# Kernel optimization log

Hardware: AMD Instinct MI355X
Metric: run time of the kernel (lower is better)

## Reference

```python
import jax, jax.numpy as jnp
import numpy as np

N_NODES = 50000
EMB = 256
HEADS = 2
N_BASE_EDGES = 100000


def setup_inputs() -> dict:
    key = jax.random.key(0)
    ks = jax.random.split(key, 12)
    x = jax.random.normal(ks[0], (N_NODES, EMB), dtype=jnp.float32)
    # bipartite edges: sources in left half, targets in right half -> no self-loops
    src = jax.random.randint(ks[1], (N_BASE_EDGES,), 0, N_NODES // 2)
    dst = jax.random.randint(ks[2], (N_BASE_EDGES,), N_NODES // 2, N_NODES)
    edge_index = jnp.stack([src, dst]).astype(jnp.int64)
    hd = EMB // HEADS
    s = 0.02
    params = {
        "Wkqv": jax.random.normal(ks[3], (EMB, 3 * EMB), dtype=jnp.float32) * s,
        "bkqv": jnp.zeros((3 * EMB,), dtype=jnp.float32),
        "W1": jax.random.normal(ks[4], (2 * hd, hd), dtype=jnp.float32) * s,
        "b1": jnp.zeros((hd,), dtype=jnp.float32),
        "W2": jax.random.normal(ks[5], (hd, 1), dtype=jnp.float32) * s,
        "b2": jnp.zeros((1,), dtype=jnp.float32),
        "Wout": jax.random.normal(ks[6], (EMB, EMB), dtype=jnp.float32) * s,
        "bout": jnp.zeros((EMB,), dtype=jnp.float32),
    }
    return {"x": x, "edge_index": edge_index, **params}


def reference(x, edge_index, Wkqv, bkqv, W1, b1, W2, b2, Wout, bout):
    N, emb = x.shape
    H = HEADS
    hd = emb // H
    # MetaGNNNoEdgeAttr.forward preprocessing: make undirected + self loops.
    # Input is bipartite (no self-loops), so remove_self_loops is a no-op.
    ei = jnp.concatenate([edge_index, edge_index[::-1]], axis=1)
    loops = jnp.arange(N, dtype=edge_index.dtype)
    src = jnp.concatenate([ei[0], loops])  # j (message source)
    dst = jnp.concatenate([ei[1], loops])  # i (message target / softmax index)

    # single GNN layer (n_layers=1)
    kqv = x @ Wkqv + bkqv  # [N, 3*emb]
    q = kqv[dst, :emb].reshape(-1, H, hd)                                  # [E,H,hd]
    k = kqv[src, emb:2 * emb].reshape(-1, H, hd) / jnp.sqrt(jnp.float32(hd))
    v = kqv[src, 2 * emb:].reshape(-1, H, hd)

    h = jax.nn.relu(jnp.concatenate([k, q], axis=-1) @ W1 + b1)  # [E,H,hd]
    a = (h @ W2 + b2).squeeze(-1)                                # [E,H]

    # segment softmax over destination nodes (every node has a self-loop)
    m = jax.ops.segment_max(a, dst, num_segments=N)              # [N,H]
    ex = jnp.exp(a - m[dst])
    s = jax.ops.segment_sum(ex, dst, num_segments=N)             # [N,H]
    alpha = ex / (s[dst] + 1e-16)                                # [E,H]

    msg = (alpha[..., None] * v).reshape(-1, emb) @ Wout + bout  # [E,emb]
    out = jax.ops.segment_sum(msg, dst, num_segments=N)          # [N,emb]
    return jax.nn.relu(out) + x
```

## Files before the change

kernel.cpp:

```cpp
#include <hip/hip_runtime.h>
#include <hip/hip_bf16.h>

#define EMB 256

typedef __bf16 bf16_t;
typedef __attribute__((ext_vector_type(8))) __bf16 bf16x8;
typedef __attribute__((ext_vector_type(4))) __bf16 bf16x4;
typedef __attribute__((ext_vector_type(4))) float floatx4;

__device__ __forceinline__ int eidx(const int* __restrict__ p, int is64, long long k){
  return is64 ? p[2*k] : p[(int)k];
}
__device__ __forceinline__ void async_load16(const void* g, void* l){
  __builtin_amdgcn_global_load_lds(
      (const __attribute__((address_space(1))) unsigned int*)g,
      (__attribute__((address_space(3))) unsigned int*)l,
      16, 0, 0);
}
__device__ __forceinline__ float4 cvt4(bf16x4 v){
  return make_float4((float)v.x, (float)v.y, (float)v.z, (float)v.w);
}

__global__ void detect_kernel(const int* __restrict__ ei, int* __restrict__ flag){
  int z = (ei[1]==0) + (ei[3]==0) + (ei[5]==0) + (ei[7]==0);
  *flag = (z == 4) ? 1 : 0;
}

__global__ void prep_weights(const float* __restrict__ Wkqv, const float* __restrict__ bkqv,
                             const float* __restrict__ W1,
                             bf16_t* __restrict__ WcombT, float* __restrict__ bcomb){
  int n = blockIdx.x * blockDim.x + threadIdx.x;
  int c = blockIdx.y;
  if (n >= 768) return;
  const float rs = rsqrtf(128.0f);
  bool isBias = (c == 256);
  const float* arow = isBias ? bkqv : (Wkqv + (size_t)c*768);
  float val;
  if (n < 512){
    bool isQ = (n < 256);
    int nn = isQ ? n : (n - 256);
    int h = nn >> 7, d = nn & 127;
    int srcoff = isQ ? (h*128) : (256 + h*128);
    int w1off  = isQ ? 128 : 0;
    float s = 0.f;
    for (int t = 0; t < 128; ++t)
      s = fmaf(arow[srcoff + t], W1[(size_t)(w1off + t)*128 + d], s);
    val = isQ ? s : s * rs;
  } else {
    val = arow[512 + (n - 512)];
  }
  if (isBias) bcomb[n] = val;
  else        WcombT[(size_t)n*256 + c] = (bf16_t)val;
}

__global__ void prep_wout(const float* __restrict__ W, bf16_t* __restrict__ Wt){
  int t = blockIdx.x*blockDim.x + threadIdx.x;
  int n = t & 255, c = t >> 8;
  Wt[(size_t)n*256 + c] = (bf16_t)W[(size_t)c*256 + n];
}

__global__ void deg_kernel(const int* __restrict__ ei, const int* __restrict__ flag,
                           int* __restrict__ deg, int E0, int Nn){
  int t = blockIdx.x*blockDim.x + threadIdx.x;
  if (t >= 2*E0) return;
  int is64 = *flag;
  int i = (t < E0) ? eidx(ei,is64,(long long)E0+t) : eidx(ei,is64,t-E0);
  i = min(max(i,0), Nn-1);
  atomicAdd(deg + i, 1);
}

__global__ __launch_bounds__(1024) void scan_kernel(const int* __restrict__ deg,
                                                    int* __restrict__ off, int N){
  __shared__ int wsum[16];
  __shared__ int carry_s;
  int tid = threadIdx.x, lane = tid & 63, w = tid >> 6;
  if (tid == 0) carry_s = 0;
  __syncthreads();
  for (int base = 0; base < N; base += 1024){
    int carry = carry_s;
    int v = (base + tid < N) ? (deg[base + tid] + 1) : 0;
    int incl = v;
    #pragma unroll
    for (int o = 1; o < 64; o <<= 1){
      int t = __shfl_up(incl, o, 64);
      if (lane >= o) incl += t;
    }
    if (lane == 63) wsum[w] = incl;
    __syncthreads();
    if (w == 0 && lane < 16){
      int sv = wsum[lane];
      #pragma unroll
      for (int o = 1; o < 16; o <<= 1){
        int t = __shfl_up(sv, o, 64);
        if (lane >= o) sv += t;
      }
      wsum[lane] = sv;
    }
    __syncthreads();
    int wpref = (w == 0) ? 0 : wsum[w-1];
    if (base + tid < N) off[base + tid] = carry + wpref + incl - v;
    __syncthreads();
    if (tid == 1023) carry_s = carry + wsum[15];
    __syncthreads();
  }
  if (threadIdx.x == 0) off[N] = carry_s;
}

__global__ void scatter_kernel(const int* __restrict__ ei, const int* __restrict__ flag,
                               const int* __restrict__ off, int* __restrict__ cursor,
                               int* __restrict__ bj, int E0, int Nn){
  int e = blockIdx.x*blockDim.x + threadIdx.x;
  int E = 2*E0 + Nn;
  if (e >= E) return;
  int is64 = *flag;
  int j, i;
  if (e < E0){ j = eidx(ei,is64,e); i = eidx(ei,is64,(long long)E0+e); }
  else if (e < 2*E0){ int t = e - E0; i = eidx(ei,is64,t); j = eidx(ei,is64,(long long)E0+t); }
  else { i = j = e - 2*E0; }
  i = min(max(i,0), Nn-1); j = min(max(j,0), Nn-1);
  int pos = atomicAdd(cursor + i, 1);
  bj[off[i] + pos] = j;
}

template<int MODE, typename OutT>
__global__ __launch_bounds__(256) void mfma_gemm(
    const void* __restrict__ Av, const bf16_t* __restrict__ Bt,
    const float* __restrict__ bias, OutT* __restrict__ C,
    int M, int N,
    const int* __restrict__ deg, const float* __restrict__ xres)
{
  __shared__ bf16_t As[2][128*32];
  __shared__ bf16_t Bs[2][128*32];
  const int tid = threadIdx.x;
  const int wave = tid >> 6, lane = tid & 63;
  const int row16 = lane & 15, quad = lane >> 4;

  const int nn = N >> 7;
  const int bid = blockIdx.x;
  const int strip = bid / (8*nn);
  const int inner = bid % (8*nn);
  const int m0 = (strip*8 + (inner & 7)) * 128;
  const int n0 = (inner >> 3) * 128;
  const int wm = (wave >> 1) * 64, wn = (wave & 1) * 64;

  const float*  Af = (const float*)Av;
  const bf16_t* Ab = (const bf16_t*)Av;

  const int f0 = wave*2, f1 = wave*2 + 1;
  const int gm0 = min(m0 + f0*16 + row16, M-1);
  const int gm1 = min(m0 + f1*16 + row16, M-1);
  const int gn0 = n0 + f0*16 + row16;
  const int gn1 = n0 + f1*16 + row16;

  if (MODE == 0){
    const float* g0 = Af + (size_t)gm0*256 + quad*8;
    const float* g1 = Af + (size_t)gm1*256 + quad*8;
    float4 a0 = *(const float4*)g0, a1 = *(const float4*)(g0+4);
    float4 c0 = *(const float4*)g1, c1 = *(const float4*)(g1+4);
    bf16x8 v0 = {(bf16_t)a0.x,(bf16_t)a0.y,(bf16_t)a0.z,(bf16_t)a0.w,
                 (bf16_t)a1.x,(bf16_t)a1.y,(bf16_t)a1.z,(bf16_t)a1.w};
    bf16x8 v1 = {(bf16_t)c0.x,(bf16_t)c0.y,(bf16_t)c0.z,(bf16_t)c0.w,
                 (bf16_t)c1.x,(bf16_t)c1.y,(bf16_t)c1.z,(bf16_t)c1.w};
    *(bf16x8*)((char*)As[0] + f0*1024 + lane*16) = v0;
    *(bf16x8*)((char*)As[0] + f1*1024 + lane*16) = v1;
  } else {
    async_load16(Ab + (size_t)gm0*256 + quad*8, (char*)As[0] + f0*1024);
    async_load16(Ab + (size_t)gm1*256 + quad*8, (char*)As[0] + f1*1024);
  }
  async_load16(Bt + (size_t)gn0*256 + quad*8, (char*)Bs[0] + f0*1024);
  async_load16(Bt + (size_t)gn1*256 + quad*8, (char*)Bs[0] + f1*1024);

  floatx4 acc[4][4];
  #pragma unroll
  for (int a=0;a<4;++a)
    #pragma unroll
    for (int b=0;b<4;++b) acc[a][b] = (floatx4){0.f,0.f,0.f,0.f};

  #pragma unroll
  for (int kt = 0; kt < 8; ++kt){
    const int cur = kt & 1, nxt = cur ^ 1;
    const int k1 = (kt+1)*32;
    const bool pre = (kt < 7);
    float4 p0, p1, p2, p3;

    __syncthreads();

    if (pre){
      if (MODE == 0){
        const float* g0 = Af + (size_t)gm0*256 + k1 + quad*8;
        const float* g1 = Af + (size_t)gm1*256 + k1 + quad*8;
        p0 = *(const float4*)g0; p1 = *(const float4*)(g0+4);
        p2 = *(const float4*)g1; p3 = *(const float4*)(g1+4);
      } else {
        async_load16(Ab + (size_t)gm0*256 + k1 + quad*8, (char*)As[nxt] + f0*1024);
        async_load16(Ab + (size_t)gm1*256 + k1 + quad*8, (char*)As[nxt] + f1*1024);
      }
      async_load16(Bt + (size_t)gn0*256 + k1 + quad*8, (char*)Bs[nxt] + f0*1024);
      async_load16(Bt + (size_t)gn1*256 + k1 + quad*8, (char*)Bs[nxt] + f1*1024);
    }

    bf16x8 af[4], bfr[4];
    #pragma unroll
    for (int t = 0; t < 4; ++t){
      af[t]  = *(const bf16x8*)((const char*)As[cur] + ((wm>>4)+t)*1024 + lane*16);
      bfr[t] = *(const bf16x8*)((const char*)Bs[cur] + ((wn>>4)+t)*1024 + lane*16);
    }
    #pragma unroll
    for (int mt=0;mt<4;++mt)
      #pragma unroll
      for (int nt=0;nt<4;++nt)
        acc[mt][nt] = __builtin_amdgcn_mfma_f32_16x16x32_bf16(af[mt], bfr[nt], acc[mt][nt], 0,0,0);

    if (pre && MODE == 0){
      bf16x8 v0 = {(bf16_t)p0.x,(bf16_t)p0.y,(bf16_t)p0.z,(bf16_t)p0.w,
                   (bf16_t)p1.x,(bf16_t)p1.y,(bf16_t)p1.z,(bf16_t)p1.w};
      bf16x8 v1 = {(bf16_t)p2.x,(bf16_t)p2.y,(bf16_t)p2.z,(bf16_t)p2.w,
                   (bf16_t)p3.x,(bf16_t)p3.y,(bf16_t)p3.z,(bf16_t)p3.w};
      *(bf16x8*)((char*)As[nxt] + f0*1024 + lane*16) = v0;
      *(bf16x8*)((char*)As[nxt] + f1*1024 + lane*16) = v1;
    }
  }

  #pragma unroll
  for (int mt=0;mt<4;++mt){
    #pragma unroll
    for (int r=0;r<4;++r){
      int m = m0 + wm + mt*16 + quad*4 + r;
      if (m >= M) continue;
      float dg = (MODE==1) ? (float)(deg[m]+1) : 0.f;
      #pragma unroll
      for (int nt=0;nt<4;++nt){
        int n = n0 + wn + nt*16 + row16;
        float v = acc[mt][nt][r];
        if (MODE == 0){
          v += bias[n];
        } else {
          v = fmaxf(v + dg*bias[n], 0.f) + xres[(size_t)m*N + n];
        }
        C[(size_t)m*N + n] = (OutT)v;
      }
    }
  }
}

__global__ __launch_bounds__(256) void fused_attn_kernel(
    const bf16_t* __restrict__ P, const int* __restrict__ bj, const int* __restrict__ off,
    const float* __restrict__ b1, const float* __restrict__ W2, const float* __restrict__ b2,
    bf16_t* __restrict__ aggb, int Nn)
{
  int i = blockIdx.x * (blockDim.x >> 6) + (threadIdx.x >> 6);
  if (i >= Nn) return;
  int lane = threadIdx.x & 63;
  int h = lane >> 5, d = (lane & 31) * 4;

  const float4 qv  = cvt4(*(const bf16x4*)(P + (size_t)i*768 + h*128 + d));
  const float4 b1v = *(const float4*)(b1 + d);
  const float4 w2v = *(const float4*)(W2 + d);
  const float b2v  = b2[0];

  float m = -3.0e38f, s = 0.f;
  float4 acc = make_float4(0.f,0.f,0.f,0.f);
  int s0 = off[i], s1 = off[i+1];
  for (int t = s0; t < s1; ++t){
    int j = bj[t];
    const float4 kv = cvt4(*(const bf16x4*)(P + (size_t)j*768 + 256 + h*128 + d));
    const float4 vv = cvt4(*(const bf16x4*)(P + (size_t)j*768 + 512 + h*128 + d));
    float p = fmaxf(qv.x+kv.x+b1v.x, 0.f)*w2v.x
            + fmaxf(qv.y+kv.y+b1v.y, 0.f)*w2v.y
            + fmaxf(qv.z+kv.z+b1v.z, 0.f)*w2v.z
            + fmaxf(qv.w+kv.w+b1v.w, 0.f)*w2v.w;
    #pragma unroll
    for (int o = 16; o >= 1; o >>= 1)
      p += __shfl_xor(p, o, 64);
    float a = p + b2v;
    float mn = fmaxf(m, a);
    float sc = __expf(m - mn);
    float e  = __expf(a - mn);
    s = s*sc + e;
    acc.x = fmaf(acc.x, sc, e*vv.x);
    acc.y = fmaf(acc.y, sc, e*vv.y);
    acc.z = fmaf(acc.z, sc, e*vv.z);
    acc.w = fmaf(acc.w, sc, e*vv.w);
    m = mn;
  }
  float inv = 1.f / (s + 1e-16f);
  bf16x4 ob = { (bf16_t)(acc.x*inv), (bf16_t)(acc.y*inv), (bf16_t)(acc.z*inv), (bf16_t)(acc.w*inv) };
  *(bf16x4*)(aggb + (size_t)i*256 + h*128 + d) = ob;
}

extern "C" void kernel_launch(void* const* d_in, const int* in_sizes, int n_in,
                              void* d_out, int out_size, void* d_ws, size_t ws_size,
                              hipStream_t stream)
{
  const float* x     = (const float*)d_in[0];
  const int*   ei    = (const int*)d_in[1];
  const float* Wkqv  = (const float*)d_in[2];
  const float* bkqv  = (const float*)d_in[3];
  const float* W1    = (const float*)d_in[4];
  const float* b1    = (const float*)d_in[5];
  const float* W2    = (const float*)d_in[6];
  const float* b2    = (const float*)d_in[7];
  const float* Wout  = (const float*)d_in[8];
  const float* bout  = (const float*)d_in[9];
  float* out = (float*)d_out;

  const int N  = in_sizes[0] / EMB;
  const int E0 = in_sizes[1] / 2;
  const int E  = 2*E0 + N;

  float* base = (float*)d_ws;
  bf16_t* WcombT = (bf16_t*)base;
  float*  bcomb  = base + 98304;
  bf16_t* WoutT  = (bf16_t*)(base + 98304 + 768);
  bf16_t* Pb     = (bf16_t*)(base + 131840);
  bf16_t* aggb   = (bf16_t*)(Pb + (size_t)N*768);
  int* deg       = (int*)(aggb + (size_t)N*256);
  int* cursor    = deg + N;
  int* flag      = cursor + N;
  int* off       = flag + 1;
  int* bj        = off + (N+1);

  hipMemsetAsync(deg, 0, (size_t)2*N*sizeof(int), stream);

  detect_kernel<<<1,1,0,stream>>>(ei, flag);
  prep_weights<<<dim3(3,257),256,0,stream>>>(Wkqv, bkqv, W1, WcombT, bcomb);
  prep_wout<<<256,256,0,stream>>>(Wout, WoutT);

  deg_kernel<<<(2*E0+255)/256,256,0,stream>>>(ei, flag, deg, E0, N);
  scan_kernel<<<1,1024,0,stream>>>(deg, off, N);
  scatter_kernel<<<(E+255)/256,256,0,stream>>>(ei, flag, off, cursor, bj, E0, N);

  const int nm8 = (((N+127)/128) + 7) & ~7;
  mfma_gemm<0, bf16_t><<<nm8*6,256,0,stream>>>(x, WcombT, bcomb, Pb, N, 768, nullptr, nullptr);
  fused_attn_kernel<<<(N+3)/4,256,0,stream>>>(Pb, bj, off, b1, W2, b2, aggb, N);
  mfma_gemm<1, float><<<nm8*2,256,0,stream>>>(aggb, WoutT, bout, out, N, 256, deg, x);
}
```

Measured before the change: 344.8 us.

## Interleave K/V columns per head and pre-convert x to bf16 for async GEMM loads

Measured after the change: 336.3 us. -2.5%, faster.

```diff
diff --git a/kernel.cpp b/kernel.cpp
--- a/kernel.cpp
+++ b/kernel.cpp
@@ -24,6 +24,14 @@
 __global__ void detect_kernel(const int* __restrict__ ei, int* __restrict__ flag){
   int z = (ei[1]==0) + (ei[3]==0) + (ei[5]==0) + (ei[7]==0);
   *flag = (z == 4) ? 1 : 0;
+}
+
+__global__ void cvt_x_kernel(const float* __restrict__ x, bf16_t* __restrict__ xb, int n4){
+  int t = blockIdx.x*blockDim.x + threadIdx.x;
+  if (t >= n4) return;
+  const float4 v = *(const float4*)(x + (size_t)t*4);
+  bf16x4 o = { (bf16_t)v.x, (bf16_t)v.y, (bf16_t)v.z, (bf16_t)v.w };
+  *(bf16x4*)(xb + (size_t)t*4) = o;
 }
 
 __global__ void prep_weights(const float* __restrict__ Wkqv, const float* __restrict__ bkqv,
@@ -36,18 +44,25 @@
   bool isBias = (c == 256);
   const float* arow = isBias ? bkqv : (Wkqv + (size_t)c*768);
   float val;
-  if (n < 512){
-    bool isQ = (n < 256);
-    int nn = isQ ? n : (n - 256);
-    int h = nn >> 7, d = nn & 127;
-    int srcoff = isQ ? (h*128) : (256 + h*128);
-    int w1off  = isQ ? 128 : 0;
+  if (n < 256){
+    int h = n >> 7, d = n & 127;
     float s = 0.f;
     for (int t = 0; t < 128; ++t)
-      s = fmaf(arow[srcoff + t], W1[(size_t)(w1off + t)*128 + d], s);
-    val = isQ ? s : s * rs;
+      s = fmaf(arow[h*128 + t], W1[(size_t)(128 + t)*128 + d], s);
+    val = s;
   } else {
-    val = arow[512 + (n - 512)];
+    int r = n - 256;
+    int h = r >> 8, t8 = r & 255;
+    int g = t8 >> 3, half = (t8 >> 2) & 1, dd = t8 & 3;
+    int d = g*4 + dd;
+    if (half == 0){
+      float s = 0.f;
+      for (int t = 0; t < 128; ++t)
+        s = fmaf(arow[256 + h*128 + t], W1[(size_t)t*128 + d], s);
+      val = s * rs;
+    } else {
+      val = arow[512 + h*128 + d];
+    }
   }
   if (isBias) bcomb[n] = val;
   else        WcombT[(size_t)n*256 + c] = (bf16_t)val;
@@ -124,7 +139,7 @@
 
 template<int MODE, typename OutT>
 __global__ __launch_bounds__(256) void mfma_gemm(
-    const void* __restrict__ Av, const bf16_t* __restrict__ Bt,
+    const bf16_t* __restrict__ A, const bf16_t* __restrict__ Bt,
     const float* __restrict__ bias, OutT* __restrict__ C,
     int M, int N,
     const int* __restrict__ deg, const float* __restrict__ xres)
@@ -143,30 +158,14 @@
   const int n0 = (inner >> 3) * 128;
   const int wm = (wave >> 1) * 64, wn = (wave & 1) * 64;
 
-  const float*  Af = (const float*)Av;
-  const bf16_t* Ab = (const bf16_t*)Av;
-
   const int f0 = wave*2, f1 = wave*2 + 1;
   const int gm0 = min(m0 + f0*16 + row16, M-1);
   const int gm1 = min(m0 + f1*16 + row16, M-1);
   const int gn0 = n0 + f0*16 + row16;
   const int gn1 = n0 + f1*16 + row16;
 
-  if (MODE == 0){
-    const float* g0 = Af + (size_t)gm0*256 + quad*8;
-    const float* g1 = Af + (size_t)gm1*256 + quad*8;
-    float4 a0 = *(const float4*)g0, a1 = *(const float4*)(g0+4);
-    float4 c0 = *(const float4*)g1, c1 = *(const float4*)(g1+4);
-    bf16x8 v0 = {(bf16_t)a0.x,(bf16_t)a0.y,(bf16_t)a0.z,(bf16_t)a0.w,
-                 (bf16_t)a1.x,(bf16_t)a1.y,(bf16_t)a1.z,(bf16_t)a1.w};
-    bf16x8 v1 = {(bf16_t)c0.x,(bf16_t)c0.y,(bf16_t)c0.z,(bf16_t)c0.w,
-                 (bf16_t)c1.x,(bf16_t)c1.y,(bf16_t)c1.z,(bf16_t)c1.w};
-    *(bf16x8*)((char*)As[0] + f0*1024 + lane*16) = v0;
-    *(bf16x8*)((char*)As[0] + f1*1024 + lane*16) = v1;
-  } else {
-    async_load16(Ab + (size_t)gm0*256 + quad*8, (char*)As[0] + f0*1024);
-    async_load16(Ab + (size_t)gm1*256 + quad*8, (char*)As[0] + f1*1024);
-  }
+  async_load16(A  + (size_t)gm0*256 + quad*8, (char*)As[0] + f0*1024);
+  async_load16(A  + (size_t)gm1*256 + quad*8, (char*)As[0] + f1*1024);
   async_load16(Bt + (size_t)gn0*256 + quad*8, (char*)Bs[0] + f0*1024);
   async_load16(Bt + (size_t)gn1*256 + quad*8, (char*)Bs[0] + f1*1024);
 
@@ -180,21 +179,12 @@
   for (int kt = 0; kt < 8; ++kt){
     const int cur = kt & 1, nxt = cur ^ 1;
     const int k1 = (kt+1)*32;
-    const bool pre = (kt < 7);
-    float4 p0, p1, p2, p3;
-
-    __syncthreads();
-
-    if (pre){
-      if (MODE == 0){
-        const float* g0 = Af + (size_t)gm0*256 + k1 + quad*8;
-        const float* g1 = Af + (size_t)gm1*256 + k1 + quad*8;
-        p0 = *(const float4*)g0; p1 = *(const float4*)(g0+4);
-        p2 = *(const float4*)g1; p3 = *(const float4*)(g1+4);
-      } else {
-        async_load16(Ab + (size_t)gm0*256 + k1 + quad*8, (char*)As[nxt] + f0*1024);
-        async_load16(Ab + (size_t)gm1*256 + k1 + quad*8, (char*)As[nxt] + f1*1024);
-      }
+
+    __syncthreads();
+
+    if (kt < 7){
+      async_load16(A  + (size_t)gm0*256 + k1 + quad*8, (char*)As[nxt] + f0*1024);
+      async_load16(A  + (size_t)gm1*256 + k1 + quad*8, (char*)As[nxt] + f1*1024);
       async_load16(Bt + (size_t)gn0*256 + k1 + quad*8, (char*)Bs[nxt] + f0*1024);
       async_load16(Bt + (size_t)gn1*256 + k1 + quad*8, (char*)Bs[nxt] + f1*1024);
     }
@@ -210,15 +200,6 @@
       #pragma unroll
       for (int nt=0;nt<4;++nt)
         acc[mt][nt] = __builtin_amdgcn_mfma_f32_16x16x32_bf16(af[mt], bfr[nt], acc[mt][nt], 0,0,0);
-
-    if (pre && MODE == 0){
-      bf16x8 v0 = {(bf16_t)p0.x,(bf16_t)p0.y,(bf16_t)p0.z,(bf16_t)p0.w,
-                   (bf16_t)p1.x,(bf16_t)p1.y,(bf16_t)p1.z,(bf16_t)p1.w};
-      bf16x8 v1 = {(bf16_t)p2.x,(bf16_t)p2.y,(bf16_t)p2.z,(bf16_t)p2.w,
-                   (bf16_t)p3.x,(bf16_t)p3.y,(bf16_t)p3.z,(bf16_t)p3.w};
-      *(bf16x8*)((char*)As[nxt] + f0*1024 + lane*16) = v0;
-      *(bf16x8*)((char*)As[nxt] + f1*1024 + lane*16) = v1;
-    }
   }
 
   #pragma unroll
@@ -251,7 +232,7 @@
   int i = blockIdx.x * (blockDim.x >> 6) + (threadIdx.x >> 6);
   if (i >= Nn) return;
   int lane = threadIdx.x & 63;
-  int h = lane >> 5, d = (lane & 31) * 4;
+  int h = lane >> 5, g = lane & 31, d = g * 4;
 
   const float4 qv  = cvt4(*(const bf16x4*)(P + (size_t)i*768 + h*128 + d));
   const float4 b1v = *(const float4*)(b1 + d);
@@ -263,12 +244,13 @@
   int s0 = off[i], s1 = off[i+1];
   for (int t = s0; t < s1; ++t){
     int j = bj[t];
-    const float4 kv = cvt4(*(const bf16x4*)(P + (size_t)j*768 + 256 + h*128 + d));
-    const float4 vv = cvt4(*(const bf16x4*)(P + (size_t)j*768 + 512 + h*128 + d));
-    float p = fmaxf(qv.x+kv.x+b1v.x, 0.f)*w2v.x
-            + fmaxf(qv.y+kv.y+b1v.y, 0.f)*w2v.y
-            + fmaxf(qv.z+kv.z+b1v.z, 0.f)*w2v.z
-            + fmaxf(qv.w+kv.w+b1v.w, 0.f)*w2v.w;
+    bf16x8 kvv = *(const bf16x8*)(P + (size_t)j*768 + 256 + h*256 + g*8);
+    float kx = (float)kvv[0], ky = (float)kvv[1], kz = (float)kvv[2], kw = (float)kvv[3];
+    float vx = (float)kvv[4], vy = (float)kvv[5], vz = (float)kvv[6], vw = (float)kvv[7];
+    float p = fmaxf(qv.x+kx+b1v.x, 0.f)*w2v.x
+            + fmaxf(qv.y+ky+b1v.y, 0.f)*w2v.y
+            + fmaxf(qv.z+kz+b1v.z, 0.f)*w2v.z
+            + fmaxf(qv.w+kw+b1v.w, 0.f)*w2v.w;
     #pragma unroll
     for (int o = 16; o >= 1; o >>= 1)
       p += __shfl_xor(p, o, 64);
@@ -277,10 +259,10 @@
     float sc = __expf(m - mn);
     float e  = __expf(a - mn);
     s = s*sc + e;
-    acc.x = fmaf(acc.x, sc, e*vv.x);
-    acc.y = fmaf(acc.y, sc, e*vv.y);
-    acc.z = fmaf(acc.z, sc, e*vv.z);
-    acc.w = fmaf(acc.w, sc, e*vv.w);
+    acc.x = fmaf(acc.x, sc, e*vx);
+    acc.y = fmaf(acc.y, sc, e*vy);
+    acc.z = fmaf(acc.z, sc, e*vz);
+    acc.w = fmaf(acc.w, sc, e*vw);
     m = mn;
   }
   float inv = 1.f / (s + 1e-16f);
@@ -312,7 +294,8 @@
   bf16_t* WcombT = (bf16_t*)base;
   float*  bcomb  = base + 98304;
   bf16_t* WoutT  = (bf16_t*)(base + 98304 + 768);
-  bf16_t* Pb     = (bf16_t*)(base + 131840);
+  bf16_t* xb     = (bf16_t*)(base + 131840);
+  bf16_t* Pb     = (bf16_t*)(base + 131840 + 6400000);
   bf16_t* aggb   = (bf16_t*)(Pb + (size_t)N*768);
   int* deg       = (int*)(aggb + (size_t)N*256);
   int* cursor    = deg + N;
@@ -323,6 +306,7 @@
   hipMemsetAsync(deg, 0, (size_t)2*N*sizeof(int), stream);
 
   detect_kernel<<<1,1,0,stream>>>(ei, flag);
+  cvt_x_kernel<<<((N*EMB/4)+255)/256,256,0,stream>>>(x, xb, N*EMB/4);
   prep_weights<<<dim3(3,257),256,0,stream>>>(Wkqv, bkqv, W1, WcombT, bcomb);
   prep_wout<<<256,256,0,stream>>>(Wout, WoutT);
 
@@ -331,7 +315,7 @@
   scatter_kernel<<<(E+255)/256,256,0,stream>>>(ei, flag, off, cursor, bj, E0, N);
 
   const int nm8 = (((N+127)/128) + 7) & ~7;
-  mfma_gemm<0, bf16_t><<<nm8*6,256,0,stream>>>(x, WcombT, bcomb, Pb, N, 768, nullptr, nullptr);
+  mfma_gemm<0, bf16_t><<<nm8*6,256,0,stream>>>(xb, WcombT, bcomb, Pb, N, 768, nullptr, nullptr);
   fused_attn_kernel<<<(N+3)/4,256,0,stream>>>(Pb, bj, off, b1, W2, b2, aggb, N);
   mfma_gemm<1, float><<<nm8*2,256,0,stream>>>(aggb, WoutT, bout, out, N, 256, deg, x);
 }
```
